# Performance work log

Measured on AMD Instinct MI355X. Metric: run time of the kernel, lower is better.

The kernel has to match this reference:

```python
import jax, jax.numpy as jnp
import numpy as np

BLOCK = 32  # 2**basic_block

def _hadamard(n):
    H = np.array([[1.0]], dtype=np.float32)
    while H.shape[0] < n:
        H = np.block([[H, H], [H, -H]])
    return H


def setup_inputs() -> dict:
    key = jax.random.key(0)
    ks = jax.random.split(key, 9)
    B, T, I, Hd, O = 64, 512, 128, 1024, 128
    sgn = lambda k, shp: jnp.where(jax.random.normal(k, shp) >= 0, 1.0, -1.0).astype(jnp.float32)
    return {
        "x": jax.random.normal(ks[0], (B, T, I), dtype=jnp.float32),
        "W_in": jax.random.normal(ks[1], (I, Hd), dtype=jnp.float32) / np.sqrt(I),
        "s1": sgn(ks[2], (Hd,)),                      # Binadamard sign vector (layer 1)
        "b1": 0.01 * jax.random.normal(ks[3], (Hd,), dtype=jnp.float32),
        "s2": sgn(ks[4], (Hd,)),                      # Binadamard sign vector (layer 2, full)
        "b2": 0.01 * jax.random.normal(ks[5], (Hd,), dtype=jnp.float32),
        "Wbn": sgn(ks[6], (Hd, Hd)) / np.sqrt(Hd),    # BinaryNorm: sign(W)/sqrt(n), materialized
        "W_out": jax.random.normal(ks[7], (Hd, O), dtype=jnp.float32) / np.sqrt(Hd),
        "b_out": jax.random.normal(ks[8], (O,), dtype=jnp.float32),
    }


def reference(x, W_in, s1, b1, s2, b2, Wbn, W_out, b_out):
    B, T, _ = x.shape
    Hd = s1.shape[0]
    Hb = jnp.asarray(_hadamard(BLOCK) / np.sqrt(BLOCK), dtype=x.dtype)   # [32,32]
    Hf = jnp.asarray(_hadamard(Hd) / np.sqrt(Hd), dtype=x.dtype)         # [Hd,Hd]
    u = jnp.einsum('bti,ih->tbh', x, W_in)  # precompute input projections, time-major

    def step(carry, u_t):
        h1, h2 = carry
        # layer 1: block-diagonal sign*Hadamard recurrence + input
        h1 = s1 * (h1.reshape(B, -1, BLOCK) @ Hb).reshape(B, Hd) + b1 + u_t
        h1b = jax.nn.relu(h1)
        # layer 2: full sign*Hadamard recurrence + binary-norm projection of h1b
        h2 = s2 * (h2 @ Hf) + b2 + h1b @ Wbn
        return (h1, h2), None

    h0 = jnp.zeros((B, Hd), dtype=x.dtype)
    (_, h2), _ = jax.lax.scan(step, (h0, h0), u)
    h2b = jax.nn.relu(h2)
    return h2b @ W_out + b_out
```

## Files before the change

### kernel.cpp

```cpp
#include <hip/hip_runtime.h>

#define B_ 64
#define T_ 512
#define I_ 128
#define H_ 1024
#define O_ 128

typedef unsigned short u16;
typedef unsigned int u32;
typedef __attribute__((ext_vector_type(8))) short short8v;
typedef __attribute__((ext_vector_type(4))) float float4v;

typedef __attribute__((address_space(1))) const void gvoid_t;
typedef __attribute__((address_space(3))) void svoid_t;

__device__ __forceinline__ u16 f2bf(float f) {
  union { float f; u32 u; } v; v.f = f;
  u32 r = v.u + 0x7FFF + ((v.u >> 16) & 1);
  return (u16)(r >> 16);
}
__device__ __forceinline__ float bf2f(u16 b) {
  union { u32 u; float f; } v; v.u = ((u32)b) << 16;
  return v.f;
}
__device__ __forceinline__ float bits2f(u32 b) {
  union { u32 u; float f; } v; v.u = b;
  return v.f;
}

__device__ __forceinline__ float fwht32(float x, int lane) {
#pragma unroll
  for (int s = 1; s <= 16; s <<= 1) {
    const float y = __shfl_xor(x, s);
    x = (lane & s) ? (y - x) : (x + y);
  }
  return x;
}

__device__ __forceinline__ void fwht32_reg(float* x) {
#pragma unroll
  for (int s = 1; s < 32; s <<= 1)
#pragma unroll
    for (int i = 0; i < 32; ++i)
      if (!(i & s)) { const float a = x[i], b = x[i | s]; x[i] = a + b; x[i | s] = a - b; }
}

__device__ __forceinline__ void transpose32(float* x, float (*T)[33], int t) {
#pragma unroll
  for (int c = 0; c < 32; ++c) T[t][c] = x[c];
#pragma unroll
  for (int c = 0; c < 32; ++c) x[c] = T[c][t];
}

__global__ __launch_bounds__(256) void prep_all(const float* __restrict__ x, const float* __restrict__ Wbn,
                                                const float* __restrict__ W_in, u16* __restrict__ xT,
                                                u16* __restrict__ WbnT, u16* __restrict__ WinT) {
  const int blk = blockIdx.x;
  if (blk < 4096) {
    const int idx = blk * 256 + threadIdx.x;
    const int n = idx >> 10, k = idx & 1023;
    WbnT[idx] = f2bf(Wbn[(size_t)k * 1024 + n]);
  } else if (blk < 4608) {
    const int idx = (blk - 4096) * 256 + threadIdx.x;
    const int n = idx >> 7, k = idx & 127;
    WinT[idx] = f2bf(W_in[(size_t)k * 1024 + n]);
  } else {
    const int idx = (blk - 4608) * 256 + threadIdx.x;
    const int i = idx & (I_ - 1);
    const int r = idx >> 7;
    const int b = r & (B_ - 1);
    const int t = r >> 6;
    xT[idx] = f2bf(x[((size_t)b * T_ + t) * I_ + i]);
  }
}

template <int K, bool BIAS>
__global__ __launch_bounds__(256) void gemm_bf16(const u16* __restrict__ A, const u16* __restrict__ Bt,
                                                 u16* __restrict__ C, const float* __restrict__ bias) {
  __shared__ u16 As[128 * 64];
  __shared__ u16 Bs[128 * 64];
  const int tid = threadIdx.x;
  const int bm = blockIdx.x, bn = blockIdx.y;
  const int lane = tid & 63, w = tid >> 6;
  const int wr = w >> 1, wc = w & 1;
  const int l16 = lane & 15, lq = lane >> 4;

  float4v acc[4][4];
#pragma unroll
  for (int mi = 0; mi < 4; ++mi)
#pragma unroll
    for (int ni = 0; ni < 4; ++ni)
#pragma unroll
      for (int j = 0; j < 4; ++j) acc[mi][ni][j] = 0.f;

  const int srow = w * 32 + (lane >> 3);
  const int scol = (((lane & 7) ^ (lane >> 3)) << 3);
  const u16* Ag = A + (size_t)(bm * 128 + srow) * K + scol;
  const u16* Bg = Bt + (size_t)(bn * 128 + srow) * K + scol;

  for (int k0 = 0; k0 < K; k0 += 64) {
    __syncthreads();
#pragma unroll
    for (int i = 0; i < 4; ++i) {
      __builtin_amdgcn_global_load_lds((gvoid_t*)(Ag + k0 + (size_t)i * 8 * K),
                                       (svoid_t*)&As[(w * 32 + i * 8) * 64], 16, 0, 0);
      __builtin_amdgcn_global_load_lds((gvoid_t*)(Bg + k0 + (size_t)i * 8 * K),
                                       (svoid_t*)&Bs[(w * 32 + i * 8) * 64], 16, 0, 0);
    }
    __syncthreads();
#pragma unroll
    for (int ks = 0; ks < 2; ++ks) {
      short8v a[4], bf[4];
#pragma unroll
      for (int mi = 0; mi < 4; ++mi) {
        const int row = wr * 64 + mi * 16 + l16;
        a[mi] = *(const short8v*)&As[row * 64 + (((ks * 4 + lq) ^ (row & 7)) << 3)];
      }
#pragma unroll
      for (int ni = 0; ni < 4; ++ni) {
        const int row = wc * 64 + ni * 16 + l16;
        bf[ni] = *(const short8v*)&Bs[row * 64 + (((ks * 4 + lq) ^ (row & 7)) << 3)];
      }
#pragma unroll
      for (int mi = 0; mi < 4; ++mi)
#pragma unroll
        for (int ni = 0; ni < 4; ++ni)
          acc[mi][ni] = __builtin_amdgcn_mfma_f32_16x16x32_bf16(a[mi], bf[ni], acc[mi][ni], 0, 0, 0);
    }
  }

#pragma unroll
  for (int mi = 0; mi < 4; ++mi)
#pragma unroll
    for (int ni = 0; ni < 4; ++ni) {
      const int row = bm * 128 + wr * 64 + mi * 16 + lq * 4;
      const int col = bn * 128 + wc * 64 + ni * 16 + l16;
      const float bv = BIAS ? bias[col] : 0.f;
#pragma unroll
      for (int j = 0; j < 4; ++j) C[(size_t)(row + j) * H_ + col] = f2bf(acc[mi][ni][j] + bv);
    }
}

__global__ __launch_bounds__(1024) void h1_Pinit(const float* __restrict__ s1, float* __restrict__ P) {
  const int hb = blockIdx.x;
  const int tid = threadIdx.x;
  const int j = tid >> 5, r = tid & 31;
  const int lane = tid & 63;
  const float sc = s1[hb * 32 + r] * 0.17677669529663687f;
  float x = (r == j) ? 1.f : 0.f;
  for (int it = 0; it < 16; ++it) x = sc * fwht32(x, lane);
  P[(size_t)hb * 1024 + r * 32 + j] = x;
}

__global__ __launch_bounds__(64) void h1_local(const u16* __restrict__ u, const float* __restrict__ s1,
                                               float* __restrict__ Ybuf) {
  const int g = blockIdx.x * 64 + threadIdx.x;
  const int hb = g & 31, b = (g >> 5) & 63, chunk = g >> 11;
  float x[32], sc[32];
#pragma unroll
  for (int i = 0; i < 32; i += 4) {
    const float4 s4 = *(const float4*)&s1[hb * 32 + i];
    sc[i] = s4.x * 0.17677669529663687f;
    sc[i + 1] = s4.y * 0.17677669529663687f;
    sc[i + 2] = s4.z * 0.17677669529663687f;
    sc[i + 3] = s4.w * 0.17677669529663687f;
  }
#pragma unroll
  for (int i = 0; i < 32; ++i) x[i] = 0.f;
  const u16* up = u + ((size_t)(chunk * 16) * B_ + b) * H_ + hb * 32;
#pragma unroll 2
  for (int k = 0; k < 16; ++k) {
    u32 wv[16];
#pragma unroll
    for (int j = 0; j < 4; ++j) {
      const uint4 t4 = *(const uint4*)(up + (size_t)k * (B_ * H_) + j * 8);
      wv[4 * j] = t4.x; wv[4 * j + 1] = t4.y; wv[4 * j + 2] = t4.z; wv[4 * j + 3] = t4.w;
    }
    fwht32_reg(x);
#pragma unroll
    for (int i2 = 0; i2 < 16; ++i2) {
      x[2 * i2]     = fmaf(sc[2 * i2],     x[2 * i2],     bits2f(wv[i2] << 16));
      x[2 * i2 + 1] = fmaf(sc[2 * i2 + 1], x[2 * i2 + 1], bits2f(wv[i2] & 0xFFFF0000u));
    }
  }
  float* yp = Ybuf + (size_t)g * 32;
#pragma unroll
  for (int i = 0; i < 32; i += 4) {
    float4 o; o.x = x[i]; o.y = x[i + 1]; o.z = x[i + 2]; o.w = x[i + 3];
    *(float4*)(yp + i) = o;
  }
}

__global__ __launch_bounds__(64) void h1_carry(const float* __restrict__ P, const float* __restrict__ Ybuf,
                                               float* __restrict__ Zbuf) {
  const int hpair = blockIdx.x, b = blockIdx.y;
  const int lane = threadIdx.x;
  const int r = lane & 31, hb = hpair * 2 + (lane >> 5);
  const float* Prow = P + (size_t)hb * 1024 + r * 32;
  float pr[32];
#pragma unroll
  for (int j = 0; j < 32; ++j) pr[j] = Prow[j];
  float z = 0.f;
  const int base = lane & 32;
  for (int c = 0; c < 32; ++c) {
    Zbuf[(((size_t)c * 64 + b) * 32 + hb) * 32 + r] = z;
    if (c < 31) {
      const float yv = Ybuf[(((size_t)c * 64 + b) * 32 + hb) * 32 + r];
      float zn = 0.f;
#pragma unroll
      for (int j = 0; j < 32; ++j) zn = fmaf(pr[j], __shfl(z, base + j), zn);
      z = zn + yv;
    }
  }
}

__global__ __launch_bounds__(64) void h1_apply(u16* __restrict__ u, const float* __restrict__ s1,
                                               const float* __restrict__ Zbuf) {
  const int g = blockIdx.x * 64 + threadIdx.x;
  const int hb = g & 31, b = (g >> 5) & 63, chunk = g >> 11;
  float x[32], sc[32];
#pragma unroll
  for (int i = 0; i < 32; i += 4) {
    const float4 s4 = *(const float4*)&s1[hb * 32 + i];
    sc[i] = s4.x * 0.17677669529663687f;
    sc[i + 1] = s4.y * 0.17677669529663687f;
    sc[i + 2] = s4.z * 0.17677669529663687f;
    sc[i + 3] = s4.w * 0.17677669529663687f;
  }
  const float* zp = Zbuf + (size_t)g * 32;
#pragma unroll
  for (int i = 0; i < 32; i += 4) {
    const float4 z4 = *(const float4*)(zp + i);
    x[i] = z4.x; x[i + 1] = z4.y; x[i + 2] = z4.z; x[i + 3] = z4.w;
  }
  u16* up = u + ((size_t)(chunk * 16) * B_ + b) * H_ + hb * 32;
#pragma unroll 2
  for (int k = 0; k < 16; ++k) {
    u32 wv[16];
#pragma unroll
    for (int j = 0; j < 4; ++j) {
      const uint4 t4 = *(const uint4*)(up + (size_t)k * (B_ * H_) + j * 8);
      wv[4 * j] = t4.x; wv[4 * j + 1] = t4.y; wv[4 * j + 2] = t4.z; wv[4 * j + 3] = t4.w;
    }
    fwht32_reg(x);
#pragma unroll
    for (int i2 = 0; i2 < 16; ++i2) {
      x[2 * i2]     = fmaf(sc[2 * i2],     x[2 * i2],     bits2f(wv[i2] << 16));
      x[2 * i2 + 1] = fmaf(sc[2 * i2 + 1], x[2 * i2 + 1], bits2f(wv[i2] & 0xFFFF0000u));
    }
    u32 ov[16];
#pragma unroll
    for (int i2 = 0; i2 < 16; ++i2) {
      const u32 lo = f2bf(fmaxf(x[2 * i2], 0.f));
      const u32 hi = f2bf(fmaxf(x[2 * i2 + 1], 0.f));
      ov[i2] = lo | (hi << 16);
    }
#pragma unroll
    for (int j = 0; j < 4; ++j) {
      uint4 t4; t4.x = ov[4 * j]; t4.y = ov[4 * j + 1]; t4.z = ov[4 * j + 2]; t4.w = ov[4 * j + 3];
      *(uint4*)(up + (size_t)k * (B_ * H_) + j * 8) = t4;
    }
  }
}

__global__ __launch_bounds__(256) void fwht_chunk(const u16* __restrict__ V, const float* __restrict__ s2,
                                                  u16* __restrict__ Bt2, u16* __restrict__ Y) {
  __shared__ float tr[4][2][32][33];
  const int wv = threadIdx.x >> 6;
  const int lane = threadIdx.x & 63;
  const int slot = lane >> 5, t = lane & 31;
  float (*T)[33] = tr[wv][slot];
  const int gs = blockIdx.x * 8 + wv * 2 + slot;

  float x[32], s0[32], s1[32];
#pragma unroll
  for (int c = 0; c < 32; ++c) {
    s0[c] = s2[t * 32 + c] * 0.03125f;
    s1[c] = s2[c * 32 + t] * 0.03125f;
  }

  if (gs < 1024) {
    const int W = gs;
#pragma unroll
    for (int c = 0; c < 32; ++c) x[c] = (t * 32 + c == W) ? 1.f : 0.f;
    for (int j = 0; j < 64; ++j) {
      if (j & 1) {
#pragma unroll
        for (int c = 0; c < 32; ++c) x[c] *= s1[c];
      } else {
#pragma unroll
        for (int c = 0; c < 32; ++c) x[c] *= s0[c];
      }
      fwht32_reg(x);
      transpose32(x, T, t);
      fwht32_reg(x);
      if (j == 31) {
        u16* dst = Bt2 + (size_t)W * 2048 + 1024 + t * 32;
        u32 ov[16];
#pragma unroll
        for (int c = 0; c < 16; ++c) ov[c] = (u32)f2bf(x[2 * c]) | ((u32)f2bf(x[2 * c + 1]) << 16);
#pragma unroll
        for (int q = 0; q < 4; ++q) {
          uint4 t4; t4.x = ov[4 * q]; t4.y = ov[4 * q + 1]; t4.z = ov[4 * q + 2]; t4.w = ov[4 * q + 3];
          *(uint4*)(dst + q * 8) = t4;
        }
      }
    }
    u16* dst = Bt2 + (size_t)W * 2048 + t * 32;
    u32 ov[16];
#pragma unroll
    for (int c = 0; c < 16; ++c) ov[c] = (u32)f2bf(x[2 * c]) | ((u32)f2bf(x[2 * c + 1]) << 16);
#pragma unroll
    for (int q = 0; q < 4; ++q) {
      uint4 t4; t4.x = ov[4 * q]; t4.y = ov[4 * q + 1]; t4.z = ov[4 * q + 2]; t4.w = ov[4 * q + 3];
      *(uint4*)(dst + q * 8) = t4;
    }
  } else {
    const int s = gs - 1024;
    const int c0 = s >> 6, b = s & 63;
    const u16* Vbase = V + ((size_t)(c0 * 32) * B_ + b) * H_;
#pragma unroll
    for (int c = 0; c < 32; ++c) x[c] = 0.f;
    for (int j = 0; j < 32; ++j) {
      const u16* vrow = Vbase + (size_t)j * (B_ * H_);
      const int pe = (j + 1) & 1;
      u32 vpk[16];
      u16 vsc[32];
      if (pe == 0) {
#pragma unroll
        for (int q = 0; q < 4; ++q) {
          const uint4 t4 = *(const uint4*)(vrow + t * 32 + q * 8);
          vpk[4 * q] = t4.x; vpk[4 * q + 1] = t4.y; vpk[4 * q + 2] = t4.z; vpk[4 * q + 3] = t4.w;
        }
      } else {
#pragma unroll
        for (int c = 0; c < 32; ++c) vsc[c] = vrow[c * 32 + t];
      }
      fwht32_reg(x);
      transpose32(x, T, t);
      fwht32_reg(x);
      if (pe == 0) {
#pragma unroll
        for (int c = 0; c < 16; ++c) {
          x[2 * c]     = fmaf(s0[2 * c],     x[2 * c],     bits2f(vpk[c] << 16));
          x[2 * c + 1] = fmaf(s0[2 * c + 1], x[2 * c + 1], bits2f(vpk[c] & 0xFFFF0000u));
        }
      } else {
#pragma unroll
        for (int c = 0; c < 32; ++c) x[c] = fmaf(s1[c], x[c], bf2f(vsc[c]));
      }
    }
    u16* dst = Y + ((size_t)c0 * B_ + b) * H_ + t * 32;
    u32 ov[16];
#pragma unroll
    for (int c = 0; c < 16; ++c) ov[c] = (u32)f2bf(x[2 * c]) | ((u32)f2bf(x[2 * c + 1]) << 16);
#pragma unroll
    for (int j = 0; j < 4; ++j) {
      uint4 t4; t4.x = ov[4 * j]; t4.y = ov[4 * j + 1]; t4.z = ov[4 * j + 2]; t4.w = ov[4 * j + 3];
      *(uint4*)(dst + j * 8) = t4;
    }
  }
}

template <bool DOUBLE, bool LAST>
__global__ __launch_bounds__(256) void combine2(const u16* __restrict__ Zold, const u16* __restrict__ Ymid,
                                                const u16* __restrict__ Yadd, const u16* __restrict__ Bt2,
                                                u16* __restrict__ Znew, float* __restrict__ h2out) {
  const int rt = blockIdx.x >> 6, nt = blockIdx.x & 63;
  const int tid = threadIdx.x;
  __shared__ float red[4][16][16];
  const int w = tid >> 6, lane = tid & 63, l16 = lane & 15, lq = lane >> 4;
  float4v acc = {0.f, 0.f, 0.f, 0.f};
  if (DOUBLE) {
    const u16* Arow = (w < 2) ? (Zold + (size_t)(rt * 16 + l16) * H_ + w * 512)
                              : (Ymid + (size_t)(rt * 16 + l16) * H_ + (w - 2) * 512);
    const u16* Ap = Arow + lq * 8;
    const u16* Bp = Bt2 + (size_t)(nt * 16 + l16) * 2048 + w * 512 + lq * 8;
#pragma unroll
    for (int ks = 0; ks < 16; ++ks) {
      short8v a = *(const short8v*)(Ap + ks * 32);
      short8v bb = *(const short8v*)(Bp + ks * 32);
      acc = __builtin_amdgcn_mfma_f32_16x16x32_bf16(a, bb, acc, 0, 0, 0);
    }
  } else {
    const u16* Ap = Zold + (size_t)(rt * 16 + l16) * H_ + w * 256 + lq * 8;
    const u16* Bp = Bt2 + (size_t)(nt * 16 + l16) * 2048 + 1024 + w * 256 + lq * 8;
#pragma unroll
    for (int ks = 0; ks < 8; ++ks) {
      short8v a = *(const short8v*)(Ap + ks * 32);
      short8v bb = *(const short8v*)(Bp + ks * 32);
      acc = __builtin_amdgcn_mfma_f32_16x16x32_bf16(a, bb, acc, 0, 0, 0);
    }
  }
#pragma unroll
  for (int j = 0; j < 4; ++j) red[w][lq * 4 + j][l16] = acc[j];
  __syncthreads();
  const int row = tid >> 4, col = tid & 15;
  float s = red[0][row][col] + red[1][row][col] + red[2][row][col] + red[3][row][col];
  const int b = rt * 16 + row, n = nt * 16 + col;
  s += bf2f(Yadd[(size_t)b * H_ + n]);
  if (LAST) h2out[(size_t)b * H_ + n] = s;
  else Znew[(size_t)b * H_ + n] = f2bf(s);
}

__global__ __launch_bounds__(128) void final_out(const float* __restrict__ h2, const float* __restrict__ W_out,
                                                 const float* __restrict__ b_out, float* __restrict__ out) {
  __shared__ float hrow[H_];
  const int b = blockIdx.x, o = threadIdx.x;
  for (int i = o; i < H_; i += 128) hrow[i] = fmaxf(h2[(size_t)b * H_ + i], 0.f);
  __syncthreads();
  float acc = b_out[o];
  for (int h = 0; h < H_; ++h) acc = fmaf(hrow[h], W_out[(size_t)h * O_ + o], acc);
  out[b * O_ + o] = acc;
}

extern "C" void kernel_launch(void* const* d_in, const int* in_sizes, int n_in,
                              void* d_out, int out_size, void* d_ws, size_t ws_size,
                              hipStream_t stream) {
  const float* x     = (const float*)d_in[0];
  const float* W_in  = (const float*)d_in[1];
  const float* s1    = (const float*)d_in[2];
  const float* b1    = (const float*)d_in[3];
  const float* s2    = (const float*)d_in[4];
  const float* b2    = (const float*)d_in[5];
  const float* Wbn   = (const float*)d_in[6];
  const float* W_out = (const float*)d_in[7];
  const float* b_out = (const float*)d_in[8];
  float* out = (float*)d_out;

  char* ws = (char*)d_ws;
  u16* u      = (u16*)ws;
  u16* V      = (u16*)(ws + 67108864);
  float* P1   = (float*)(ws + 67108864);
  float* Zbuf = (float*)(ws + 69206016);
  u16* xT     = (u16*)(ws + 134217728);
  float* Ybuf = (float*)(ws + 134217728);
  u16* WbnT   = (u16*)(ws + 142606336);
  u16* WinT   = (u16*)(ws + 144703488);
  u16* Bt2    = (u16*)(ws + 134217728);
  u16* Y      = (u16*)(ws + 138412032);
  u16* Zb0    = (u16*)(ws + 140509184);
  u16* Zb1    = (u16*)(ws + 140640256);
  float* h2   = (float*)(ws + 140771328);

  prep_all<<<20992, 256, 0, stream>>>(x, Wbn, W_in, xT, WbnT, WinT);
  h1_Pinit<<<32, 1024, 0, stream>>>(s1, P1);
  gemm_bf16<128, true><<<dim3(256, 8), 256, 0, stream>>>(xT, WinT, u, b1);
  h1_local<<<1024, 64, 0, stream>>>(u, s1, Ybuf);
  h1_carry<<<dim3(16, 64), 64, 0, stream>>>(P1, Ybuf, Zbuf);
  h1_apply<<<1024, 64, 0, stream>>>(u, s1, Zbuf);
  gemm_bf16<1024, true><<<dim3(256, 8), 256, 0, stream>>>(u, WbnT, V, b2);
  fwht_chunk<<<256, 256, 0, stream>>>(V, s2, Bt2, Y);

  const size_t BH = (size_t)B_ * H_;
  combine2<true, false><<<256, 256, 0, stream>>>(Y,            Y + 1 * BH,  Y + 2 * BH,  Bt2, Zb0, nullptr);
  combine2<true, false><<<256, 256, 0, stream>>>(Zb0,          Y + 3 * BH,  Y + 4 * BH,  Bt2, Zb1, nullptr);
  combine2<true, false><<<256, 256, 0, stream>>>(Zb1,          Y + 5 * BH,  Y + 6 * BH,  Bt2, Zb0, nullptr);
  combine2<true, false><<<256, 256, 0, stream>>>(Zb0,          Y + 7 * BH,  Y + 8 * BH,  Bt2, Zb1, nullptr);
  combine2<true, false><<<256, 256, 0, stream>>>(Zb1,          Y + 9 * BH,  Y + 10 * BH, Bt2, Zb0, nullptr);
  combine2<true, false><<<256, 256, 0, stream>>>(Zb0,          Y + 11 * BH, Y + 12 * BH, Bt2, Zb1, nullptr);
  combine2<true, false><<<256, 256, 0, stream>>>(Zb1,          Y + 13 * BH, Y + 14 * BH, Bt2, Zb0, nullptr);
  combine2<false, true><<<256, 256, 0, stream>>>(Zb0,          nullptr,     Y + 15 * BH, Bt2, nullptr, h2);

  final_out<<<64, 128, 0, stream>>>(h2, W_out, b_out, out);
}
```

Measured before the change: 331.1 us.

## Fuse combine chain and output projection into one persistent kernel with grid barriers

Replaces eight combine2 launches plus final_out with a single 256-block persistent kernel that syncs between steps through atomic-counter grid barriers, and splits the output matvec across two thread halves. Also rewrites the weight transposes in prep_all as 32x32 shared-memory tiled transposes, so both reads and writes are coalesced. The aim is to remove per-launch overhead and uncoalesced transpose traffic. It relies on all 256 blocks being co-resident and needs a memset of the barrier counters on every call.

```diff
diff --git a/kernel.cpp b/kernel.cpp
--- a/kernel.cpp
+++ b/kernel.cpp
@@ -55,17 +55,40 @@
 __global__ __launch_bounds__(256) void prep_all(const float* __restrict__ x, const float* __restrict__ Wbn,
                                                 const float* __restrict__ W_in, u16* __restrict__ xT,
                                                 u16* __restrict__ WbnT, u16* __restrict__ WinT) {
+  __shared__ float tl[32][33];
   const int blk = blockIdx.x;
-  if (blk < 4096) {
-    const int idx = blk * 256 + threadIdx.x;
-    const int n = idx >> 10, k = idx & 1023;
-    WbnT[idx] = f2bf(Wbn[(size_t)k * 1024 + n]);
-  } else if (blk < 4608) {
-    const int idx = (blk - 4096) * 256 + threadIdx.x;
-    const int n = idx >> 7, k = idx & 127;
-    WinT[idx] = f2bf(W_in[(size_t)k * 1024 + n]);
+  const int tid = threadIdx.x;
+  if (blk < 1024) {
+    const int bx = blk & 31, by = blk >> 5;
+    const int c = tid & 31, r8 = tid >> 5;
+#pragma unroll
+    for (int i = 0; i < 4; ++i) {
+      const int r = r8 + i * 8;
+      tl[r][c] = Wbn[(size_t)(by * 32 + r) * 1024 + bx * 32 + c];
+    }
+    __syncthreads();
+#pragma unroll
+    for (int i = 0; i < 4; ++i) {
+      const int r = r8 + i * 8;
+      WbnT[(size_t)(bx * 32 + r) * 1024 + by * 32 + c] = f2bf(tl[c][r]);
+    }
+  } else if (blk < 1152) {
+    const int t2 = blk - 1024;
+    const int bx = t2 & 31, by = t2 >> 5;
+    const int c = tid & 31, r8 = tid >> 5;
+#pragma unroll
+    for (int i = 0; i < 4; ++i) {
+      const int r = r8 + i * 8;
+      tl[r][c] = W_in[(size_t)(by * 32 + r) * 1024 + bx * 32 + c];
+    }
+    __syncthreads();
+#pragma unroll
+    for (int i = 0; i < 4; ++i) {
+      const int r = r8 + i * 8;
+      WinT[(size_t)(bx * 32 + r) * 128 + by * 32 + c] = f2bf(tl[c][r]);
+    }
   } else {
-    const int idx = (blk - 4608) * 256 + threadIdx.x;
+    const int idx = (blk - 1152) * 256 + tid;
     const int i = idx & (I_ - 1);
     const int r = idx >> 7;
     const int b = r & (B_ - 1);
@@ -362,16 +385,39 @@
   }
 }
 
-template <bool DOUBLE, bool LAST>
-__global__ __launch_bounds__(256) void combine2(const u16* __restrict__ Zold, const u16* __restrict__ Ymid,
-                                                const u16* __restrict__ Yadd, const u16* __restrict__ Bt2,
-                                                u16* __restrict__ Znew, float* __restrict__ h2out) {
-  const int rt = blockIdx.x >> 6, nt = blockIdx.x & 63;
+__device__ __forceinline__ void gridbar(int* bar, int idx) {
+  __threadfence();
+  __syncthreads();
+  if (threadIdx.x == 0) {
+    __hip_atomic_fetch_add(&bar[idx], 1, __ATOMIC_RELAXED, __HIP_MEMORY_SCOPE_AGENT);
+    while (__hip_atomic_load(&bar[idx], __ATOMIC_RELAXED, __HIP_MEMORY_SCOPE_AGENT) < 256) {
+      __builtin_amdgcn_s_sleep(1);
+    }
+  }
+  __syncthreads();
+  __threadfence();
+}
+
+__global__ __launch_bounds__(256) void h2_tail(const u16* __restrict__ Y, const u16* __restrict__ Bt2,
+                                               u16* __restrict__ Zb0, u16* __restrict__ Zb1,
+                                               float* __restrict__ h2, const float* __restrict__ W_out,
+                                               const float* __restrict__ b_out, float* __restrict__ out,
+                                               int* __restrict__ bar) {
+  __shared__ float red[4][16][16];
+  const int blk = blockIdx.x;
   const int tid = threadIdx.x;
-  __shared__ float red[4][16][16];
+  const int rt = blk >> 6, nt = blk & 63;
   const int w = tid >> 6, lane = tid & 63, l16 = lane & 15, lq = lane >> 4;
-  float4v acc = {0.f, 0.f, 0.f, 0.f};
-  if (DOUBLE) {
+  const int row = tid >> 4, col = tid & 15;
+  const size_t BH = (size_t)B_ * H_;
+
+  const u16* Zold = Y;
+  u16* zo[2] = {Zb0, Zb1};
+  for (int step = 0; step < 7; ++step) {
+    const u16* Ymid = Y + (size_t)(2 * step + 1) * BH;
+    const u16* Yadd = Y + (size_t)(2 * step + 2) * BH;
+    u16* Znew = zo[step & 1];
+    float4v acc = {0.f, 0.f, 0.f, 0.f};
     const u16* Arow = (w < 2) ? (Zold + (size_t)(rt * 16 + l16) * H_ + w * 512)
                               : (Ymid + (size_t)(rt * 16 + l16) * H_ + (w - 2) * 512);
     const u16* Ap = Arow + lq * 8;
@@ -382,7 +428,17 @@
       short8v bb = *(const short8v*)(Bp + ks * 32);
       acc = __builtin_amdgcn_mfma_f32_16x16x32_bf16(a, bb, acc, 0, 0, 0);
     }
-  } else {
+#pragma unroll
+    for (int j = 0; j < 4; ++j) red[w][lq * 4 + j][l16] = acc[j];
+    __syncthreads();
+    float s = red[0][row][col] + red[1][row][col] + red[2][row][col] + red[3][row][col];
+    s += bf2f(Yadd[(size_t)(rt * 16 + row) * H_ + nt * 16 + col]);
+    Znew[(size_t)(rt * 16 + row) * H_ + nt * 16 + col] = f2bf(s);
+    gridbar(bar, step);
+    Zold = Znew;
+  }
+  {
+    float4v acc = {0.f, 0.f, 0.f, 0.f};
     const u16* Ap = Zold + (size_t)(rt * 16 + l16) * H_ + w * 256 + lq * 8;
     const u16* Bp = Bt2 + (size_t)(nt * 16 + l16) * 2048 + 1024 + w * 256 + lq * 8;
 #pragma unroll
@@ -391,27 +447,25 @@
       short8v bb = *(const short8v*)(Bp + ks * 32);
       acc = __builtin_amdgcn_mfma_f32_16x16x32_bf16(a, bb, acc, 0, 0, 0);
     }
-  }
-#pragma unroll
-  for (int j = 0; j < 4; ++j) red[w][lq * 4 + j][l16] = acc[j];
-  __syncthreads();
-  const int row = tid >> 4, col = tid & 15;
-  float s = red[0][row][col] + red[1][row][col] + red[2][row][col] + red[3][row][col];
-  const int b = rt * 16 + row, n = nt * 16 + col;
-  s += bf2f(Yadd[(size_t)b * H_ + n]);
-  if (LAST) h2out[(size_t)b * H_ + n] = s;
-  else Znew[(size_t)b * H_ + n] = f2bf(s);
-}
-
-__global__ __launch_bounds__(128) void final_out(const float* __restrict__ h2, const float* __restrict__ W_out,
-                                                 const float* __restrict__ b_out, float* __restrict__ out) {
-  __shared__ float hrow[H_];
-  const int b = blockIdx.x, o = threadIdx.x;
-  for (int i = o; i < H_; i += 128) hrow[i] = fmaxf(h2[(size_t)b * H_ + i], 0.f);
-  __syncthreads();
-  float acc = b_out[o];
-  for (int h = 0; h < H_; ++h) acc = fmaf(hrow[h], W_out[(size_t)h * O_ + o], acc);
-  out[b * O_ + o] = acc;
+#pragma unroll
+    for (int j = 0; j < 4; ++j) red[w][lq * 4 + j][l16] = acc[j];
+    __syncthreads();
+    float s = red[0][row][col] + red[1][row][col] + red[2][row][col] + red[3][row][col];
+    s += bf2f(Y[(size_t)15 * BH + (size_t)(rt * 16 + row) * H_ + nt * 16 + col]);
+    h2[(size_t)(rt * 16 + row) * H_ + nt * 16 + col] = s;
+    gridbar(bar, 7);
+  }
+  if (blk < 64) {
+    const int o = tid & 127, half = tid >> 7;
+    float acc = 0.f;
+    const float* hrow = h2 + (size_t)blk * H_ + half * 512;
+    const float* wp = W_out + (size_t)(half * 512) * O_ + o;
+    for (int h = 0; h < 512; ++h) acc = fmaf(fmaxf(hrow[h], 0.f), wp[(size_t)h * O_], acc);
+    float* rr = (float*)red;
+    if (half) rr[o] = acc;
+    __syncthreads();
+    if (!half) out[blk * O_ + o] = acc + rr[o] + b_out[o];
+  }
 }
 
 extern "C" void kernel_launch(void* const* d_in, const int* in_sizes, int n_in,
@@ -442,8 +496,10 @@
   u16* Zb0    = (u16*)(ws + 140509184);
   u16* Zb1    = (u16*)(ws + 140640256);
   float* h2   = (float*)(ws + 140771328);
-
-  prep_all<<<20992, 256, 0, stream>>>(x, Wbn, W_in, xT, WbnT, WinT);
+  int* bar    = (int*)(ws + 144965632);
+
+  hipMemsetAsync((void*)bar, 0, 64, stream);
+  prep_all<<<17536, 256, 0, stream>>>(x, Wbn, W_in, xT, WbnT, WinT);
   h1_Pinit<<<32, 1024, 0, stream>>>(s1, P1);
   gemm_bf16<128, true><<<dim3(256, 8), 256, 0, stream>>>(xT, WinT, u, b1);
   h1_local<<<1024, 64, 0, stream>>>(u, s1, Ybuf);
@@ -451,16 +507,5 @@
   h1_apply<<<1024, 64, 0, stream>>>(u, s1, Zbuf);
   gemm_bf16<1024, true><<<dim3(256, 8), 256, 0, stream>>>(u, WbnT, V, b2);
   fwht_chunk<<<256, 256, 0, stream>>>(V, s2, Bt2, Y);
-
-  const size_t BH = (size_t)B_ * H_;
-  combine2<true, false><<<256, 256, 0, stream>>>(Y,            Y + 1 * BH,  Y + 2 * BH,  Bt2, Zb0, nullptr);
-  combine2<true, false><<<256, 256, 0, stream>>>(Zb0,          Y + 3 * BH,  Y + 4 * BH,  Bt2, Zb1, nullptr);
-  combine2<true, false><<<256, 256, 0, stream>>>(Zb1,          Y + 5 * BH,  Y + 6 * BH,  Bt2, Zb0, nullptr);
-  combine2<true, false><<<256, 256, 0, stream>>>(Zb0,          Y + 7 * BH,  Y + 8 * BH,  Bt2, Zb1, nullptr);
-  combine2<true, false><<<256, 256, 0, stream>>>(Zb1,          Y + 9 * BH,  Y + 10 * BH, Bt2, Zb0, nullptr);
-  combine2<true, false><<<256, 256, 0, stream>>>(Zb0,          Y + 11 * BH, Y + 12 * BH, Bt2, Zb1, nullptr);
-  combine2<true, false><<<256, 256, 0, stream>>>(Zb1,          Y + 13 * BH, Y + 14 * BH, Bt2, Zb0, nullptr);
-  combine2<false, true><<<256, 256, 0, stream>>>(Zb0,          nullptr,     Y + 15 * BH, Bt2, nullptr, h2);
-
-  final_out<<<64, 128, 0, stream>>>(h2, W_out, b_out, out);
-}
+  h2_tail<<<256, 256, 0, stream>>>(Y, Bt2, Zb0, Zb1, h2, W_out, b_out, out, bar);
+}
```

New measurement: 646.9 us. 95.4% more time.
